# Performance work log

Hardware: AMD Instinct MI355X
Metric: run time of the kernel (lower is better)

The kernel has to match this reference:

```python
import jax, jax.numpy as jnp
import numpy as np

D_MODEL = 1024
N_HEADS = 16
D_K = D_MODEL // N_HEADS
D_FF = 4 * D_MODEL
LN_EPS = 1e-5


def _layer_norm(x, gamma, beta):
    mu = jnp.mean(x, axis=-1, keepdims=True)
    var = jnp.mean(jnp.square(x - mu), axis=-1, keepdims=True)
    return (x - mu) * jax.lax.rsqrt(var + LN_EPS) * gamma + beta


def setup_inputs() -> dict:
    key = jax.random.key(0)
    ks = jax.random.split(key, 16)
    s = 1.0 / np.sqrt(D_MODEL)
    sf = 1.0 / np.sqrt(D_FF)
    return {
        "x": jax.random.normal(ks[0], (4, 2048, D_MODEL), dtype=jnp.float32),
        "ln1_g": jnp.ones((D_MODEL,), jnp.float32),
        "ln1_b": jnp.zeros((D_MODEL,), jnp.float32),
        "ln2_g": jnp.ones((D_MODEL,), jnp.float32),
        "ln2_b": jnp.zeros((D_MODEL,), jnp.float32),
        "Wq": jax.random.uniform(ks[1], (D_MODEL, D_MODEL), jnp.float32, -s, s),
        "bq": jax.random.uniform(ks[2], (D_MODEL,), jnp.float32, -s, s),
        "Wk": jax.random.uniform(ks[3], (D_MODEL, D_MODEL), jnp.float32, -s, s),
        "bk": jax.random.uniform(ks[4], (D_MODEL,), jnp.float32, -s, s),
        "Wv": jax.random.uniform(ks[5], (D_MODEL, D_MODEL), jnp.float32, -s, s),
        "bv": jax.random.uniform(ks[6], (D_MODEL,), jnp.float32, -s, s),
        "Wo": jax.random.uniform(ks[7], (D_MODEL, D_MODEL), jnp.float32, -s, s),
        "bo": jax.random.uniform(ks[8], (D_MODEL,), jnp.float32, -s, s),
        "W1": jax.random.uniform(ks[9], (D_MODEL, D_FF), jnp.float32, -s, s),
        "b1": jax.random.uniform(ks[10], (D_FF,), jnp.float32, -s, s),
        "W2": jax.random.uniform(ks[11], (D_FF, D_MODEL), jnp.float32, -sf, sf),
        "b2": jax.random.uniform(ks[12], (D_MODEL,), jnp.float32, -sf, sf),
    }


def reference(x, ln1_g, ln1_b, ln2_g, ln2_b, Wq, bq, Wk, bk, Wv, bv, Wo, bo, W1, b1, W2, b2):
    B, S, _ = x.shape
    # --- pre-LN multi-head attention (dropout=0, mask=None) ---
    xn = _layer_norm(x, ln1_g, ln1_b)                      # [B,S,D]
    q = (xn @ Wq + bq).reshape(B, S, N_HEADS, D_K)          # [B,S,H,Dk]
    k = (xn @ Wk + bk).reshape(B, S, N_HEADS, D_K)
    v = (xn @ Wv + bv).reshape(B, S, N_HEADS, D_K)
    scores = jnp.einsum("bqhd,bkhd->bhqk", q, k) / np.sqrt(D_K)  # [B,H,S,S]
    attn = jax.nn.softmax(scores, axis=-1)
    ctx = jnp.einsum("bhqk,bkhd->bqhd", attn, v).reshape(B, S, D_MODEL)
    x = x + (ctx @ Wo + bo)
    # --- pre-LN FFN ---
    xn = _layer_norm(x, ln2_g, ln2_b)
    h = jax.nn.relu(xn @ W1 + b1)                           # [B,S,4D]
    x = x + (h @ W2 + b2)
    return x
```

## Files before the change

### kernel.cpp

```cpp
#include <hip/hip_runtime.h>
#include <cstdint>

typedef unsigned short u16;
typedef unsigned int u32;
typedef __bf16 bf16x8 __attribute__((ext_vector_type(8)));
typedef float f32x4 __attribute__((ext_vector_type(4)));
typedef u16 u16x8 __attribute__((ext_vector_type(8)));

#define GLOBAL_AS __attribute__((address_space(1)))
#define LDS_AS __attribute__((address_space(3)))

__device__ __forceinline__ u16 f2b(float f) {
  u32 u = __builtin_bit_cast(u32, f);
  u += 0x7fffu + ((u >> 16) & 1u);
  return (u16)(u >> 16);
}

__global__ void transpose_cvt(const float* __restrict__ in, u16* __restrict__ out,
                              int K, int N) {
  __shared__ float tile[32][33];
  const int tx = threadIdx.x, ty = threadIdx.y;
  const int n0 = blockIdx.x * 32, k0 = blockIdx.y * 32;
#pragma unroll
  for (int i = 0; i < 4; i++)
    tile[ty + i * 8][tx] = in[(size_t)(k0 + ty + i * 8) * N + n0 + tx];
  __syncthreads();
#pragma unroll
  for (int i = 0; i < 4; i++)
    out[(size_t)(n0 + ty + i * 8) * K + k0 + tx] = f2b(tile[tx][ty + i * 8]);
}

__global__ __launch_bounds__(256) void ln_fwd(const float* __restrict__ x,
                                              const float* __restrict__ gamma,
                                              const float* __restrict__ beta,
                                              u16* __restrict__ out) {
  const int wid = threadIdx.x >> 6, lane = threadIdx.x & 63;
  const size_t row = (size_t)blockIdx.x * 4 + wid;
  const float* xr = x + row * 1024;
  float4 v[4];
  float s = 0.f, s2 = 0.f;
#pragma unroll
  for (int i = 0; i < 4; i++) {
    v[i] = *(const float4*)(xr + i * 256 + lane * 4);
    s += v[i].x + v[i].y + v[i].z + v[i].w;
    s2 += v[i].x * v[i].x + v[i].y * v[i].y + v[i].z * v[i].z + v[i].w * v[i].w;
  }
#pragma unroll
  for (int m = 1; m < 64; m <<= 1) {
    s += __shfl_xor(s, m);
    s2 += __shfl_xor(s2, m);
  }
  const float mu = s * (1.f / 1024.f);
  const float var = s2 * (1.f / 1024.f) - mu * mu;
  const float rs = rsqrtf(var + 1e-5f);
  u16* orow = out + row * 1024;
#pragma unroll
  for (int i = 0; i < 4; i++) {
    float4 gv = *(const float4*)(gamma + i * 256 + lane * 4);
    float4 bv = *(const float4*)(beta + i * 256 + lane * 4);
    float y0 = (v[i].x - mu) * rs * gv.x + bv.x;
    float y1 = (v[i].y - mu) * rs * gv.y + bv.y;
    float y2 = (v[i].z - mu) * rs * gv.z + bv.z;
    float y3 = (v[i].w - mu) * rs * gv.w + bv.w;
    uint2 pk;
    pk.x = (u32)f2b(y0) | ((u32)f2b(y1) << 16);
    pk.y = (u32)f2b(y2) | ((u32)f2b(y3) << 16);
    *(uint2*)(orow + i * 256 + lane * 4) = pk;
  }
}

template <int MODE>
__global__ __launch_bounds__(256) void gemm_bt(
    const u16* __restrict__ A, const u16* __restrict__ BT,
    const float* __restrict__ b0, const float* __restrict__ b1,
    const float* __restrict__ b2, const float* __restrict__ res,
    void* __restrict__ outp, int M, int N, int K) {
  __shared__ __align__(16) u16 Alds[128 * 64];
  __shared__ __align__(16) u16 Blds[128 * 64];
  const int tid = threadIdx.x;
  const int wid = tid >> 6, lane = tid & 63;
  const int wm = wid >> 1, wn = wid & 1;
  const int g = lane >> 4, l15 = lane & 15;
  const int bm = blockIdx.y * 128, bn = blockIdx.x * 128;

  f32x4 acc[4][4] = {};

  const int srow = wid * 32 + (lane >> 3);
  const int scol = (lane & 7) * 8;
  const u16* Ag = A + (size_t)(bm + srow) * K + scol;
  const u16* Bg = BT + (size_t)(bn + srow) * K + scol;

  for (int k0 = 0; k0 < K; k0 += 64) {
    __syncthreads();
#pragma unroll
    for (int i = 0; i < 4; i++)
      __builtin_amdgcn_global_load_lds(
          (const GLOBAL_AS u32*)(Ag + (size_t)(i * 8) * K + k0),
          (LDS_AS u32*)&Alds[(wid * 32 + i * 8) * 64], 16, 0, 0);
#pragma unroll
    for (int i = 0; i < 4; i++)
      __builtin_amdgcn_global_load_lds(
          (const GLOBAL_AS u32*)(Bg + (size_t)(i * 8) * K + k0),
          (LDS_AS u32*)&Blds[(wid * 32 + i * 8) * 64], 16, 0, 0);
    __syncthreads();
#pragma unroll
    for (int ks = 0; ks < 2; ks++) {
      bf16x8 af[4], bfr[4];
#pragma unroll
      for (int mt = 0; mt < 4; mt++)
        af[mt] = *(const bf16x8*)&Alds[(wm * 64 + mt * 16 + l15) * 64 + ks * 32 + g * 8];
#pragma unroll
      for (int nt = 0; nt < 4; nt++)
        bfr[nt] = *(const bf16x8*)&Blds[(wn * 64 + nt * 16 + l15) * 64 + ks * 32 + g * 8];
#pragma unroll
      for (int mt = 0; mt < 4; mt++)
#pragma unroll
        for (int nt = 0; nt < 4; nt++)
          acc[mt][nt] = __builtin_amdgcn_mfma_f32_16x16x32_bf16(
              af[mt], bfr[nt], acc[mt][nt], 0, 0, 0);
    }
  }

  const float* bias = b0;
  float scale = 1.f;
  if (MODE == 0) {
    bias = (bn < 1024) ? b0 : (bn < 2048 ? b1 : b2);
    if (bn < 1024) scale = 0.18033688011112042f;
  }
#pragma unroll
  for (int mt = 0; mt < 4; mt++) {
#pragma unroll
    for (int nt = 0; nt < 4; nt++) {
      const int orow = bm + wm * 64 + mt * 16 + g * 4;
      const int ocol = bn + wn * 64 + nt * 16 + l15;
      const float bv = bias[MODE == 0 ? (ocol & 1023) : ocol];
#pragma unroll
      for (int r = 0; r < 4; r++) {
        const float v = acc[mt][nt][r] + bv;
        const size_t oi = (size_t)(orow + r) * N + ocol;
        if (MODE == 0)
          ((u16*)outp)[oi] = f2b(v * scale);
        else if (MODE == 1)
          ((u16*)outp)[oi] = f2b(v > 0.f ? v : 0.f);
        else
          ((float*)outp)[oi] = v + res[oi];
      }
    }
  }
}

__global__ __launch_bounds__(256) void attn_fwd(const u16* __restrict__ QKV,
                                                u16* __restrict__ ctx) {
  __shared__ __align__(16) u16 Klds[64 * 64];
  __shared__ __align__(16) u16 Vt[64 * 64];
  __shared__ __align__(16) u16 Plds[4][16 * 64];
  const int tid = threadIdx.x;
  const int wid = tid >> 6, lane = tid & 63;
  const int g = lane >> 4, l15 = lane & 15, l7 = lane & 7;
  const int qt = blockIdx.x, h = blockIdx.y, b = blockIdx.z;

  const u16* Qbase = QKV + (size_t)(b * 2048 + qt * 64 + wid * 16) * 3072 + h * 64;
  bf16x8 qf[2];
#pragma unroll
  for (int ks = 0; ks < 2; ks++)
    qf[ks] = *(const bf16x8*)(Qbase + (size_t)l15 * 3072 + ks * 32 + g * 8);

  const u16* Kg = QKV + (size_t)(b * 2048) * 3072 + 1024 + h * 64;
  const u16* Vg = QKV + (size_t)(b * 2048) * 3072 + 2048 + h * 64;

  float mrun[4], lrun[4];
  f32x4 cacc[4] = {};
#pragma unroll
  for (int r = 0; r < 4; r++) {
    mrun[r] = -3.0e38f;
    lrun[r] = 0.f;
  }

  const int skv0 = (tid & 31) * 2, sd0 = (tid >> 5) * 8;

  for (int t = 0; t < 32; t++) {
    __syncthreads();
#pragma unroll
    for (int i = 0; i < 2; i++) {
      const int c = tid + 256 * i;
      const int kv = c >> 3, dg = c & 7;
      u16x8 kval = *(const u16x8*)(Kg + (size_t)(t * 64 + kv) * 3072 + dg * 8);
      *(u16x8*)&Klds[kv * 64 + ((dg ^ (kv & 7)) << 3)] = kval;
    }
    {
      u16x8 v0 = *(const u16x8*)(Vg + (size_t)(t * 64 + skv0) * 3072 + sd0);
      u16x8 v1 = *(const u16x8*)(Vg + (size_t)(t * 64 + skv0 + 1) * 3072 + sd0);
#pragma unroll
      for (int i = 0; i < 8; i++) {
        const int d = sd0 + i;
        const u32 pack = (u32)v0[i] | ((u32)v1[i] << 16);
        *(u32*)&Vt[d * 64 + (((skv0 >> 3) ^ (d & 7)) << 3) + (skv0 & 7)] = pack;
      }
    }
    __syncthreads();
    f32x4 s[4] = {};
#pragma unroll
    for (int nt = 0; nt < 4; nt++) {
      const int kv = nt * 16 + l15;
#pragma unroll
      for (int ks = 0; ks < 2; ks++) {
        const int dg = ks * 4 + g;
        bf16x8 kf = *(const bf16x8*)&Klds[kv * 64 + ((dg ^ (kv & 7)) << 3)];
        s[nt] = __builtin_amdgcn_mfma_f32_16x16x32_bf16(qf[ks], kf, s[nt], 0, 0, 0);
      }
    }
    float pm[4];
#pragma unroll
    for (int r = 0; r < 4; r++)
      pm[r] = fmaxf(fmaxf(s[0][r], s[1][r]), fmaxf(s[2][r], s[3][r]));
#pragma unroll
    for (int m = 1; m < 16; m <<= 1)
#pragma unroll
      for (int r = 0; r < 4; r++) pm[r] = fmaxf(pm[r], __shfl_xor(pm[r], m));
    float alpha[4], psum[4];
#pragma unroll
    for (int r = 0; r < 4; r++) {
      const float mn = fmaxf(mrun[r], pm[r]);
      alpha[r] = exp2f(mrun[r] - mn);
      mrun[r] = mn;
      psum[r] = 0.f;
    }
#pragma unroll
    for (int nt = 0; nt < 4; nt++) {
      const int col = nt * 16 + l15, cg = col >> 3;
#pragma unroll
      for (int r = 0; r < 4; r++) {
        const float p = exp2f(s[nt][r] - mrun[r]);
        psum[r] += p;
        const int prow = g * 4 + r;
        Plds[wid][prow * 64 + ((cg ^ (prow & 7)) << 3) + (col & 7)] = f2b(p);
      }
    }
#pragma unroll
    for (int m = 1; m < 16; m <<= 1)
#pragma unroll
      for (int r = 0; r < 4; r++) psum[r] += __shfl_xor(psum[r], m);
#pragma unroll
    for (int r = 0; r < 4; r++) lrun[r] = lrun[r] * alpha[r] + psum[r];
#pragma unroll
    for (int dt = 0; dt < 4; dt++)
#pragma unroll
      for (int r = 0; r < 4; r++) cacc[dt][r] *= alpha[r];
    asm volatile("s_waitcnt lgkmcnt(0)" ::: "memory");
#pragma unroll
    for (int ks = 0; ks < 2; ks++) {
      bf16x8 pf = *(const bf16x8*)&Plds[wid][l15 * 64 + (((ks * 4 + g) ^ l7) << 3)];
#pragma unroll
      for (int dt = 0; dt < 4; dt++) {
        const int d = dt * 16 + l15;
        const int kg = ks * 4 + g;
        bf16x8 vf = *(const bf16x8*)&Vt[d * 64 + ((kg ^ (d & 7)) << 3)];
        cacc[dt] = __builtin_amdgcn_mfma_f32_16x16x32_bf16(pf, vf, cacc[dt], 0, 0, 0);
      }
    }
  }
#pragma unroll
  for (int r = 0; r < 4; r++) {
    const float inv = 1.f / lrun[r];
    const int orow = b * 2048 + qt * 64 + wid * 16 + g * 4 + r;
#pragma unroll
    for (int dt = 0; dt < 4; dt++) {
      const int ocol = h * 64 + dt * 16 + l15;
      ctx[(size_t)orow * 1024 + ocol] = f2b(cacc[dt][r] * inv);
    }
  }
}

extern "C" void kernel_launch(void* const* d_in, const int* in_sizes, int n_in,
                              void* d_out, int out_size, void* d_ws, size_t ws_size,
                              hipStream_t stream) {
  const float* x = (const float*)d_in[0];
  const float* ln1g = (const float*)d_in[1];
  const float* ln1b = (const float*)d_in[2];
  const float* ln2g = (const float*)d_in[3];
  const float* ln2b = (const float*)d_in[4];
  const float* Wq = (const float*)d_in[5];
  const float* bq = (const float*)d_in[6];
  const float* Wk = (const float*)d_in[7];
  const float* bk = (const float*)d_in[8];
  const float* Wv = (const float*)d_in[9];
  const float* bv = (const float*)d_in[10];
  const float* Wo = (const float*)d_in[11];
  const float* bo = (const float*)d_in[12];
  const float* W1 = (const float*)d_in[13];
  const float* b1 = (const float*)d_in[14];
  const float* W2 = (const float*)d_in[15];
  const float* b2 = (const float*)d_in[16];

  char* ws = (char*)d_ws;
  u16* WqkvT = (u16*)(ws + 0);
  u16* WoT = (u16*)(ws + 6291456);
  u16* W1T = (u16*)(ws + 8388608);
  u16* W2T = (u16*)(ws + 16777216);
  u16* xn = (u16*)(ws + 25165824);
  float* x2 = (float*)(ws + 41943040);
  u16* ctx = (u16*)(ws + 75497472);
  u16* big = (u16*)(ws + 92274688);
  u16* QKVb = big;
  u16* hbuf = big;
  float* outF = (float*)d_out;

  const dim3 tb(32, 8);
  transpose_cvt<<<dim3(32, 32), tb, 0, stream>>>(Wq, WqkvT, 1024, 1024);
  transpose_cvt<<<dim3(32, 32), tb, 0, stream>>>(Wk, WqkvT + 1024 * 1024, 1024, 1024);
  transpose_cvt<<<dim3(32, 32), tb, 0, stream>>>(Wv, WqkvT + 2048 * 1024, 1024, 1024);
  transpose_cvt<<<dim3(32, 32), tb, 0, stream>>>(Wo, WoT, 1024, 1024);
  transpose_cvt<<<dim3(128, 32), tb, 0, stream>>>(W1, W1T, 1024, 4096);
  transpose_cvt<<<dim3(32, 128), tb, 0, stream>>>(W2, W2T, 4096, 1024);

  ln_fwd<<<dim3(2048), dim3(256), 0, stream>>>(x, ln1g, ln1b, xn);
  gemm_bt<0><<<dim3(24, 64), dim3(256), 0, stream>>>(xn, WqkvT, bq, bk, bv, nullptr,
                                                     (void*)QKVb, 8192, 3072, 1024);
  attn_fwd<<<dim3(32, 16, 4), dim3(256), 0, stream>>>(QKVb, ctx);
  gemm_bt<2><<<dim3(8, 64), dim3(256), 0, stream>>>(ctx, WoT, bo, nullptr, nullptr, x,
                                                    (void*)x2, 8192, 1024, 1024);
  ln_fwd<<<dim3(2048), dim3(256), 0, stream>>>(x2, ln2g, ln2b, xn);
  gemm_bt<1><<<dim3(32, 64), dim3(256), 0, stream>>>(xn, W1T, b1, nullptr, nullptr,
                                                     nullptr, (void*)hbuf, 8192, 4096, 1024);
  gemm_bt<2><<<dim3(8, 64), dim3(256), 0, stream>>>(hbuf, W2T, b2, nullptr, nullptr, x2,
                                                    (void*)outF, 8192, 1024, 4096);
}
```

Before: 715.6 us.

## Double-buffer attention K/V via direct global-to-LDS loads and keep P in registers

Rewrites the flash-attention kernel to prefetch the next K/V tile with global_load_lds into a second LDS buffer while the current tile is computed. It computes S transposed so each lane holds a full query column, keeping P in registers as packed bf16 for a 16x16x16 MFMA, which removes the P LDS round trip and most shuffles. V fragments are read with ds_read_b64_tr_b16 transposing loads, so the manual V transpose is gone. This adds hardcoded swizzle and lgkmcnt assumptions that are fragile, and it doubles LDS use per block.

```diff
diff --git a/kernel.cpp b/kernel.cpp
--- a/kernel.cpp
+++ b/kernel.cpp
@@ -6,6 +6,7 @@
 typedef __bf16 bf16x8 __attribute__((ext_vector_type(8)));
 typedef float f32x4 __attribute__((ext_vector_type(4)));
 typedef u16 u16x8 __attribute__((ext_vector_type(8)));
+typedef u32 u32x2 __attribute__((ext_vector_type(2)));
 
 #define GLOBAL_AS __attribute__((address_space(1)))
 #define LDS_AS __attribute__((address_space(3)))
@@ -151,12 +152,11 @@
 
 __global__ __launch_bounds__(256) void attn_fwd(const u16* __restrict__ QKV,
                                                 u16* __restrict__ ctx) {
-  __shared__ __align__(16) u16 Klds[64 * 64];
-  __shared__ __align__(16) u16 Vt[64 * 64];
-  __shared__ __align__(16) u16 Plds[4][16 * 64];
+  __shared__ __align__(16) u16 Klds[2][64 * 64];
+  __shared__ __align__(16) u16 Vlds[2][64 * 64];
   const int tid = threadIdx.x;
   const int wid = tid >> 6, lane = tid & 63;
-  const int g = lane >> 4, l15 = lane & 15, l7 = lane & 7;
+  const int g = lane >> 4, l15 = lane & 15;
   const int qt = blockIdx.x, h = blockIdx.y, b = blockIdx.z;
 
   const u16* Qbase = QKV + (size_t)(b * 2048 + qt * 64 + wid * 16) * 3072 + h * 64;
@@ -168,106 +168,126 @@
   const u16* Kg = QKV + (size_t)(b * 2048) * 3072 + 1024 + h * 64;
   const u16* Vg = QKV + (size_t)(b * 2048) * 3072 + 2048 + h * 64;
 
-  float mrun[4], lrun[4];
+  int kvK[2], colK[2], kvV[2], d0V[2];
+#pragma unroll
+  for (int i = 0; i < 2; i++) {
+    const int p = tid + 256 * i;
+    kvK[i] = p >> 3;
+    colK[i] = ((p & 7) ^ (kvK[i] & 7)) << 3;
+    kvV[i] = ((p >> 5) << 2) | ((p >> 1) & 3);
+    d0V[i] = (((p >> 3) & 3) << 4) | ((p & 1) << 3);
+  }
+
+#define STAGE(bufidx, tt)                                                          \
+  do {                                                                             \
+    const size_t roff = (size_t)(tt) * 64 * 3072;                                  \
+    _Pragma("unroll") for (int i = 0; i < 2; i++) {                                \
+      __builtin_amdgcn_global_load_lds(                                            \
+          (const GLOBAL_AS u32*)(Kg + roff + (size_t)kvK[i] * 3072 + colK[i]),     \
+          (LDS_AS u32*)&Klds[bufidx][(i * 256 + wid * 64) * 8], 16, 0, 0);         \
+      __builtin_amdgcn_global_load_lds(                                            \
+          (const GLOBAL_AS u32*)(Vg + roff + (size_t)kvV[i] * 3072 + d0V[i]),      \
+          (LDS_AS u32*)&Vlds[bufidx][(i * 256 + wid * 64) * 8], 16, 0, 0);         \
+    }                                                                              \
+  } while (0)
+
+#define TRISSUE(dst, dtc)                                                          \
+  do {                                                                             \
+    _Pragma("unroll") for (int nt = 0; nt < 4; nt++) {                             \
+      const u32 a_ = vb + (u32)((((nt * 4 + g) * 4 + (dtc)) << 7) + (l15 << 1));   \
+      asm volatile("ds_read_b64_tr_b16 %0, %1" : "=v"(dst[nt]) : "v"(a_)           \
+                   : "memory");                                                    \
+    }                                                                              \
+  } while (0)
+
+  float mrun = -3.0e38f, lrun = 0.f;
   f32x4 cacc[4] = {};
-#pragma unroll
-  for (int r = 0; r < 4; r++) {
-    mrun[r] = -3.0e38f;
-    lrun[r] = 0.f;
-  }
-
-  const int skv0 = (tid & 31) * 2, sd0 = (tid >> 5) * 8;
-
+
+  STAGE(0, 0);
+  int cur = 0;
   for (int t = 0; t < 32; t++) {
     __syncthreads();
-#pragma unroll
-    for (int i = 0; i < 2; i++) {
-      const int c = tid + 256 * i;
-      const int kv = c >> 3, dg = c & 7;
-      u16x8 kval = *(const u16x8*)(Kg + (size_t)(t * 64 + kv) * 3072 + dg * 8);
-      *(u16x8*)&Klds[kv * 64 + ((dg ^ (kv & 7)) << 3)] = kval;
-    }
-    {
-      u16x8 v0 = *(const u16x8*)(Vg + (size_t)(t * 64 + skv0) * 3072 + sd0);
-      u16x8 v1 = *(const u16x8*)(Vg + (size_t)(t * 64 + skv0 + 1) * 3072 + sd0);
-#pragma unroll
-      for (int i = 0; i < 8; i++) {
-        const int d = sd0 + i;
-        const u32 pack = (u32)v0[i] | ((u32)v1[i] << 16);
-        *(u32*)&Vt[d * 64 + (((skv0 >> 3) ^ (d & 7)) << 3) + (skv0 & 7)] = pack;
-      }
-    }
-    __syncthreads();
-    f32x4 s[4] = {};
+    if (t < 31) STAGE(cur ^ 1, t + 1);
+
+    const u16* Kc = &Klds[cur][0];
+    f32x4 s4[4] = {};
 #pragma unroll
     for (int nt = 0; nt < 4; nt++) {
       const int kv = nt * 16 + l15;
+      const int sw = kv & 7;
 #pragma unroll
       for (int ks = 0; ks < 2; ks++) {
-        const int dg = ks * 4 + g;
-        bf16x8 kf = *(const bf16x8*)&Klds[kv * 64 + ((dg ^ (kv & 7)) << 3)];
-        s[nt] = __builtin_amdgcn_mfma_f32_16x16x32_bf16(qf[ks], kf, s[nt], 0, 0, 0);
+        bf16x8 kf = *(const bf16x8*)&Kc[kv * 64 + (((ks * 4 + g) ^ sw) << 3)];
+        s4[nt] = __builtin_amdgcn_mfma_f32_16x16x32_bf16(kf, qf[ks], s4[nt], 0, 0, 0);
       }
     }
-    float pm[4];
-#pragma unroll
-    for (int r = 0; r < 4; r++)
-      pm[r] = fmaxf(fmaxf(s[0][r], s[1][r]), fmaxf(s[2][r], s[3][r]));
-#pragma unroll
-    for (int m = 1; m < 16; m <<= 1)
-#pragma unroll
-      for (int r = 0; r < 4; r++) pm[r] = fmaxf(pm[r], __shfl_xor(pm[r], m));
-    float alpha[4], psum[4];
-#pragma unroll
-    for (int r = 0; r < 4; r++) {
-      const float mn = fmaxf(mrun[r], pm[r]);
-      alpha[r] = exp2f(mrun[r] - mn);
-      mrun[r] = mn;
-      psum[r] = 0.f;
-    }
+
+    float pm = s4[0][0];
+#pragma unroll
+    for (int nt = 0; nt < 4; nt++)
+#pragma unroll
+      for (int r = 0; r < 4; r++) pm = fmaxf(pm, s4[nt][r]);
+    pm = fmaxf(pm, __shfl_xor(pm, 16));
+    pm = fmaxf(pm, __shfl_xor(pm, 32));
+    const float mn = fmaxf(mrun, pm);
+    const float alpha = exp2f(mrun - mn);
+    mrun = mn;
+
+    float psum = 0.f;
+    u32 w[4][2];
 #pragma unroll
     for (int nt = 0; nt < 4; nt++) {
-      const int col = nt * 16 + l15, cg = col >> 3;
-#pragma unroll
-      for (int r = 0; r < 4; r++) {
-        const float p = exp2f(s[nt][r] - mrun[r]);
-        psum[r] += p;
-        const int prow = g * 4 + r;
-        Plds[wid][prow * 64 + ((cg ^ (prow & 7)) << 3) + (col & 7)] = f2b(p);
+      const float p0 = exp2f(s4[nt][0] - mn);
+      const float p1 = exp2f(s4[nt][1] - mn);
+      const float p2 = exp2f(s4[nt][2] - mn);
+      const float p3 = exp2f(s4[nt][3] - mn);
+      psum += (p0 + p1) + (p2 + p3);
+      asm("v_cvt_pk_bf16_f32 %0, %1, %2" : "=v"(w[nt][0]) : "v"(p0), "v"(p1));
+      asm("v_cvt_pk_bf16_f32 %0, %1, %2" : "=v"(w[nt][1]) : "v"(p2), "v"(p3));
+    }
+    psum += __shfl_xor(psum, 16);
+    psum += __shfl_xor(psum, 32);
+    lrun = lrun * alpha + psum;
+#pragma unroll
+    for (int dt = 0; dt < 4; dt++) cacc[dt] *= alpha;
+
+    const u32 vb = (u32)(uintptr_t)(const LDS_AS u16*)&Vlds[cur][0];
+    u32x2 vf[2][4];
+    TRISSUE(vf[0], 0);
+#pragma unroll
+    for (int dt = 0; dt < 4; dt++) {
+      if (dt < 3) TRISSUE(vf[(dt + 1) & 1], dt + 1);
+      if (dt < 3)
+        asm volatile("s_waitcnt lgkmcnt(4)" ::: "memory");
+      else
+        asm volatile("s_waitcnt lgkmcnt(0)" ::: "memory");
+      __builtin_amdgcn_sched_barrier(0);
+#pragma unroll
+      for (int nt = 0; nt < 4; nt++) {
+        const u32x2 pf = {w[nt][0], w[nt][1]};
+        asm volatile("v_mfma_f32_16x16x16_bf16 %0, %1, %2, %0"
+                     : "+v"(cacc[dt])
+                     : "v"(vf[dt & 1][nt]), "v"(pf));
       }
     }
-#pragma unroll
-    for (int m = 1; m < 16; m <<= 1)
-#pragma unroll
-      for (int r = 0; r < 4; r++) psum[r] += __shfl_xor(psum[r], m);
-#pragma unroll
-    for (int r = 0; r < 4; r++) lrun[r] = lrun[r] * alpha[r] + psum[r];
-#pragma unroll
-    for (int dt = 0; dt < 4; dt++)
-#pragma unroll
-      for (int r = 0; r < 4; r++) cacc[dt][r] *= alpha[r];
-    asm volatile("s_waitcnt lgkmcnt(0)" ::: "memory");
-#pragma unroll
-    for (int ks = 0; ks < 2; ks++) {
-      bf16x8 pf = *(const bf16x8*)&Plds[wid][l15 * 64 + (((ks * 4 + g) ^ l7) << 3)];
-#pragma unroll
-      for (int dt = 0; dt < 4; dt++) {
-        const int d = dt * 16 + l15;
-        const int kg = ks * 4 + g;
-        bf16x8 vf = *(const bf16x8*)&Vt[d * 64 + ((kg ^ (d & 7)) << 3)];
-        cacc[dt] = __builtin_amdgcn_mfma_f32_16x16x32_bf16(pf, vf, cacc[dt], 0, 0, 0);
-      }
-    }
-  }
-#pragma unroll
-  for (int r = 0; r < 4; r++) {
-    const float inv = 1.f / lrun[r];
-    const int orow = b * 2048 + qt * 64 + wid * 16 + g * 4 + r;
-#pragma unroll
-    for (int dt = 0; dt < 4; dt++) {
-      const int ocol = h * 64 + dt * 16 + l15;
-      ctx[(size_t)orow * 1024 + ocol] = f2b(cacc[dt][r] * inv);
-    }
+    cur ^= 1;
+  }
+#undef STAGE
+#undef TRISSUE
+
+  asm volatile("s_nop 7" :::);
+  asm volatile("s_nop 7" :::);
+
+  const float inv = 1.f / lrun;
+  u16* op = ctx + (size_t)(b * 2048 + qt * 64 + wid * 16 + l15) * 1024 + h * 64 + g * 4;
+#pragma unroll
+  for (int dt = 0; dt < 4; dt++) {
+    u32 lo, hi;
+    const float c0 = cacc[dt][0] * inv, c1 = cacc[dt][1] * inv;
+    const float c2 = cacc[dt][2] * inv, c3 = cacc[dt][3] * inv;
+    asm("v_cvt_pk_bf16_f32 %0, %1, %2" : "=v"(lo) : "v"(c0), "v"(c1));
+    asm("v_cvt_pk_bf16_f32 %0, %1, %2" : "=v"(hi) : "v"(c2), "v"(c3));
+    *(u32x2*)(op + dt * 16) = (u32x2){lo, hi};
   }
 }
 
```

New measurement: 618.6 us. 13.6% less time.
